# Optimization experiments

Hardware: AMD Instinct MI355X
Metric: run time of the kernel (lower is better)

## Reference

```python
import jax, jax.numpy as jnp
import numpy as np

NUM_ITER = 64
M_CONST = jnp.array([-1.0, 1.0], dtype=jnp.float32)      # constellation m
ALPHA   = jnp.array([0.5, 0.5], dtype=jnp.float32)       # prior alpha


def setup_inputs() -> dict:
    key = jax.random.key(0)
    k1, k2, k3 = jax.random.split(key, 3)
    B, N_RX, N_TX = 16384, 64, 32
    # channel matrix, scaled ~1/sqrt(N_rx) like a normalized MIMO channel
    Ht = jax.random.normal(k1, (B, N_RX, N_TX), dtype=jnp.float32) / jnp.sqrt(jnp.float32(N_RX))
    yt = jax.random.normal(k2, (B, N_RX), dtype=jnp.float32)
    sigmat0 = jax.random.uniform(k3, (B,), dtype=jnp.float32, minval=0.1, maxval=0.6)
    taui = jnp.ones((NUM_ITER + 1,), dtype=jnp.float32)          # taui0 = 1
    delta = jnp.full((NUM_ITER,), 0.01, dtype=jnp.float32)       # small step size for stability
    return {"yt": yt, "Ht": Ht, "sigmat0": sigmat0, "taui": taui, "delta": delta}


def _cmdnet(yt, Ht, sigmat0, taui, delta):
    m = M_CONST                      # [M]
    log_alpha = jnp.log(ALPHA)       # [M]
    sig2 = (sigmat0 ** 2)[:, None, None]          # [B,1,1]
    B, _, K = Ht.shape
    M = m.shape[0]

    # G0 = zeros broadcast to [B, K, M]
    G = jnp.zeros((B, K, M), dtype=Ht.dtype)
    tau = jnp.abs(taui[0])
    ft = jax.nn.softmax((log_alpha + G) * tau, axis=-1)   # [B,K,M]
    xt = jnp.sum(ft * m, axis=-1)                         # [B,K]

    HH = jnp.einsum('bnk,bnl->bkl', Ht, Ht)               # [B,K,K]
    yH = jnp.einsum('bn,bnk->bk', yt, Ht)                 # [B,K]

    def step(carry, xs):
        G, ft, xt, tau = carry
        d_i, tau_next = xs
        xHH = jnp.einsum('bk,bkl->bl', xt, HH)            # [B,K]
        grad_x = tau * (ft * m - ft * xt[..., None])      # [B,K,M]
        grad_L = sig2 * (1.0 - jnp.exp(-G)) + grad_x * (xHH - yH)[..., None]
        G = G - d_i * grad_L
        tau = jnp.abs(tau_next)
        ft = jax.nn.softmax((log_alpha + G) * tau, axis=-1)
        xt = jnp.sum(ft * m, axis=-1)
        return (G, ft, xt, tau), None

    (G, ft, xt, tau), _ = jax.lax.scan(step, (G, ft, xt, tau), (delta, taui[1:]))
    return ft, xt


def reference(yt, Ht, sigmat0, taui, delta):
    return _cmdnet(yt, Ht, sigmat0, taui, delta)
```

## Files before the change

kernel.cpp:

```cpp
#include <hip/hip_runtime.h>


#define NRX 64
#define KSYM 32

typedef float  f32x16 __attribute__((ext_vector_type(16)));
typedef short  short8 __attribute__((ext_vector_type(8)));

__device__ __forceinline__ float readlane_f(float v, int lane) {
    return __int_as_float(__builtin_amdgcn_readlane(__float_as_int(v), lane));
}
__device__ __forceinline__ unsigned cvt_pk_bf16(float a, float b) {
    unsigned r;
    asm("v_cvt_pk_bf16_f32 %0, %1, %2" : "=v"(r) : "v"(a), "v"(b));
    return r;
}
template <int N>
__device__ __forceinline__ float dpp_ror_f(float v) {
    return __int_as_float(__builtin_amdgcn_update_dpp(
        0, __float_as_int(v), 0x120 + N, 0xF, 0xF, true));
}
template <int N>
__device__ __forceinline__ int dpp_ror_i(int v) {
    return __builtin_amdgcn_update_dpp(0, v, 0x120 + N, 0xF, 0xF, true);
}

union FragU { unsigned u[4]; short8 s; };

__global__ __launch_bounds__(256, 4) void cmdnet_kernel(
    const float* __restrict__ yt,
    const float* __restrict__ Ht,
    const float* __restrict__ sigmat0,
    const float* __restrict__ taui,
    const float* __restrict__ delta,
    float* __restrict__ out_ft,
    float* __restrict__ out_xt,
    int niter)
{
    __shared__ __align__(16) float hhbuf[4][KSYM * KSYM];
    __shared__ __align__(16) float ytL[4][2][NRX];

    const int tid  = threadIdx.x;
    const int w    = tid >> 6;
    const int lane = tid & 63;
    const int k    = lane & 31;
    const int h    = lane >> 5;
    const int hi8  = h * 8;
    const int bb   = blockIdx.x * 8 + w * 2;
    const int b    = bb + h;

    ytL[w][0][lane] = yt[(size_t)bb * NRX + lane];
    ytL[w][1][lane] = yt[(size_t)bb * NRX + NRX + lane];

    float dreg = 0.f, treg = 1.f;
    if (lane < niter) { dreg = delta[lane]; treg = fabsf(taui[lane + 1]); }

    float sig2 = sigmat0[b];
    sig2 *= sig2;

    f32x16 acc0, acc1;
    #pragma unroll
    for (int j = 0; j < 16; ++j) { acc0[j] = 0.f; acc1[j] = 0.f; }
    float yhp0 = 0.f, yhp1 = 0.f;

    #pragma unroll
    for (int s = 0; s < 2; ++s) {
        const float* Hb = Ht + ((size_t)(bb + s)) * (NRX * KSYM);
        #pragma unroll
        for (int c = 0; c < 4; ++c) {
            const float* base = Hb + (c * 16 + hi8) * KSYM + k;
            float f[8];
            #pragma unroll
            for (int e = 0; e < 8; ++e) f[e] = base[e * KSYM];

            float4 ya = *reinterpret_cast<const float4*>(&ytL[w][s][c * 16 + hi8]);
            float4 yb = *reinterpret_cast<const float4*>(&ytL[w][s][c * 16 + hi8 + 4]);
            float yp = (s == 0) ? yhp0 : yhp1;
            yp = fmaf(ya.x, f[0], yp); yp = fmaf(ya.y, f[1], yp);
            yp = fmaf(ya.z, f[2], yp); yp = fmaf(ya.w, f[3], yp);
            yp = fmaf(yb.x, f[4], yp); yp = fmaf(yb.y, f[5], yp);
            yp = fmaf(yb.z, f[6], yp); yp = fmaf(yb.w, f[7], yp);
            if (s == 0) yhp0 = yp; else yhp1 = yp;

            FragU hiF, loF;
            #pragma unroll
            for (int p = 0; p < 4; ++p) {
                unsigned hp = cvt_pk_bf16(f[2*p], f[2*p+1]);
                float h0 = __uint_as_float(hp << 16);
                float h1 = __uint_as_float(hp & 0xffff0000u);
                loF.u[p] = cvt_pk_bf16(f[2*p] - h0, f[2*p+1] - h1);
                hiF.u[p] = hp;
            }
            if (s == 0) {
                acc0 = __builtin_amdgcn_mfma_f32_32x32x16_bf16(hiF.s, hiF.s, acc0, 0, 0, 0);
                acc0 = __builtin_amdgcn_mfma_f32_32x32x16_bf16(hiF.s, loF.s, acc0, 0, 0, 0);
                acc0 = __builtin_amdgcn_mfma_f32_32x32x16_bf16(loF.s, hiF.s, acc0, 0, 0, 0);
            } else {
                acc1 = __builtin_amdgcn_mfma_f32_32x32x16_bf16(hiF.s, hiF.s, acc1, 0, 0, 0);
                acc1 = __builtin_amdgcn_mfma_f32_32x32x16_bf16(hiF.s, loF.s, acc1, 0, 0, 0);
                acc1 = __builtin_amdgcn_mfma_f32_32x32x16_bf16(loF.s, hiF.s, acc1, 0, 0, 0);
            }
        }
    }

    float yh0 = yhp0 + __shfl_xor(yhp0, 32, 64);
    float yh1 = yhp1 + __shfl_xor(yhp1, 32, 64);
    float yh  = h ? yh1 : yh0;

    float own_d[32];
    const int low4 = k & 15;
    float* buf = &hhbuf[w][0];
    #pragma unroll
    for (int s = 0; s < 2; ++s) {
        #pragma unroll
        for (int j = 0; j < 16; ++j) {
            int row = (j & 3) + 8 * (j >> 2) + 4 * h;
            buf[row * 32 + k] = s ? acc1[j] : acc0[j];
        }
        if (h == s) {
            const float* rowp = buf + k * 32;
            own_d[0]  = rowp[k];
            own_d[16] = rowp[k ^ 16];
            #define GATH(J) { \
                int idx = dpp_ror_i<J>(low4); \
                own_d[J]        = rowp[(k & 16) | idx]; \
                own_d[16 + (J)] = rowp[((k & 16) ^ 16) | idx]; }
            GATH(1)  GATH(2)  GATH(3)  GATH(4)  GATH(5)
            GATH(6)  GATH(7)  GATH(8)  GATH(9)  GATH(10)
            GATH(11) GATH(12) GATH(13) GATH(14) GATH(15)
            #undef GATH
        }
    }

    float tau = fabsf(taui[0]);
    float G0 = 0.f, G1 = 0.f;
    float ft0 = 0.5f, ft1 = 0.5f, xt = 0.f;

    for (int i = 0; i < niter; ++i) {
        float d        = readlane_f(dreg, i);
        float tau_next = readlane_f(treg, i);

        float xts = __shfl_xor(xt, 16, 64);
        float a[4];
        a[0] = fmaf(own_d[0], xt, -yh);
        a[1] = own_d[16] * xts;
        a[2] = 0.f; a[3] = 0.f;
        #define STEP(J) { \
            float ra = dpp_ror_f<J>(xt); \
            float rb = dpp_ror_f<J>(xts); \
            a[(J) & 3]       = fmaf(own_d[J],        ra, a[(J) & 3]); \
            a[((J) + 2) & 3] = fmaf(own_d[16 + (J)], rb, a[((J) + 2) & 3]); }
        STEP(1)  STEP(2)  STEP(3)  STEP(4)  STEP(5)
        STEP(6)  STEP(7)  STEP(8)  STEP(9)  STEP(10)
        STEP(11) STEP(12) STEP(13) STEP(14) STEP(15)
        #undef STEP
        float r = (a[0] + a[1]) + (a[2] + a[3]);

        float p  = 2.f * tau * ft0 * ft1 * r;
        float e0 = __expf(-G0);
        float e1 = __expf(-G1);
        float g0 = fmaf(sig2, 1.f - e0, -p);
        float g1 = fmaf(sig2, 1.f - e1,  p);
        G0 = fmaf(-d, g0, G0);
        G1 = fmaf(-d, g1, G1);

        tau = tau_next;
        float z  = tau * (G1 - G0);
        float ez = __expf(-fabsf(z));
        float sg = __builtin_amdgcn_rcpf(1.f + ez);
        float abig = sg, asml = ez * sg;
        bool ps = (z >= 0.f);
        ft1 = ps ? abig : asml;
        ft0 = ps ? asml : abig;
        xt  = ft1 - ft0;
    }

    float2 f2 = make_float2(ft0, ft1);
    reinterpret_cast<float2*>(out_ft)[(size_t)b * KSYM + k] = f2;
    out_xt[(size_t)b * KSYM + k] = xt;
}

extern "C" void kernel_launch(void* const* d_in, const int* in_sizes, int n_in,
                              void* d_out, int out_size, void* d_ws, size_t ws_size,
                              hipStream_t stream) {
    const float* yt    = (const float*)d_in[0];
    const float* Ht    = (const float*)d_in[1];
    const float* sg    = (const float*)d_in[2];
    const float* taui  = (const float*)d_in[3];
    const float* delta = (const float*)d_in[4];
    int B     = in_sizes[2];
    int niter = in_sizes[4];
    float* out    = (float*)d_out;
    float* out_ft = out;
    float* out_xt = out + (size_t)B * 64;

    dim3 grid(B / 8), block(256);
    hipLaunchKernelGGL(cmdnet_kernel, grid, block, 0, stream,
                       yt, Ht, sg, taui, delta, out_ft, out_xt, niter);
}
```

Before: 87.74 us.

## Pack Gram matrix to fp16 and use fma_mix in iteration loop

Stores each lane's 32 Gram-matrix entries as 16 packed fp16 pairs and computes the xHH matvec with v_fma_mix_f32, rotating a single packed register per step instead of two floats. It also swaps the shfl_xor for ds_swizzle, rewrites the softmax update in terms of xt alone (ft0*ft1 = (1-xt^2)/4, xt = tanh-like form), and raises the occupancy hint to 8 blocks per CU by scoping the accumulator per batch. This halves register pressure and DPP traffic in the latency-bound loop, at the cost of fp16 rounding of HH and xt, which may affect accuracy over 64 iterations.

```diff
diff --git a/kernel.cpp b/kernel.cpp
--- a/kernel.cpp
+++ b/kernel.cpp
@@ -15,19 +15,21 @@
     asm("v_cvt_pk_bf16_f32 %0, %1, %2" : "=v"(r) : "v"(a), "v"(b));
     return r;
 }
-template <int N>
-__device__ __forceinline__ float dpp_ror_f(float v) {
-    return __int_as_float(__builtin_amdgcn_update_dpp(
-        0, __float_as_int(v), 0x120 + N, 0xF, 0xF, true));
+__device__ __forceinline__ int cvt_pk_f16(float a, float b) {
+    int r;
+    asm("v_cvt_pkrtz_f16_f32 %0, %1, %2" : "=v"(r) : "v"(a), "v"(b));
+    return r;
 }
 template <int N>
 __device__ __forceinline__ int dpp_ror_i(int v) {
     return __builtin_amdgcn_update_dpp(0, v, 0x120 + N, 0xF, 0xF, true);
 }
+#define MIXLO(acc, o, x) asm("v_fma_mix_f32 %0, %1, %2, %0 op_sel:[0,0,0] op_sel_hi:[1,1,0]" : "+v"(acc) : "v"(o), "v"(x))
+#define MIXHI(acc, o, x) asm("v_fma_mix_f32 %0, %1, %2, %0 op_sel:[1,1,0] op_sel_hi:[1,1,0]" : "+v"(acc) : "v"(o), "v"(x))
 
 union FragU { unsigned u[4]; short8 s; };
 
-__global__ __launch_bounds__(256, 4) void cmdnet_kernel(
+__global__ __launch_bounds__(256, 8) void cmdnet_kernel(
     const float* __restrict__ yt,
     const float* __restrict__ Ht,
     const float* __restrict__ sigmat0,
@@ -58,13 +60,17 @@
     float sig2 = sigmat0[b];
     sig2 *= sig2;
 
-    f32x16 acc0, acc1;
-    #pragma unroll
-    for (int j = 0; j < 16; ++j) { acc0[j] = 0.f; acc1[j] = 0.f; }
+    float* buf = &hhbuf[w][0];
+    const int low4 = k & 15;
+    int own_pk[16];
     float yhp0 = 0.f, yhp1 = 0.f;
 
     #pragma unroll
     for (int s = 0; s < 2; ++s) {
+        f32x16 acc;
+        #pragma unroll
+        for (int j = 0; j < 16; ++j) acc[j] = 0.f;
+
         const float* Hb = Ht + ((size_t)(bb + s)) * (NRX * KSYM);
         #pragma unroll
         for (int c = 0; c < 4; ++c) {
@@ -91,15 +97,26 @@
                 loF.u[p] = cvt_pk_bf16(f[2*p] - h0, f[2*p+1] - h1);
                 hiF.u[p] = hp;
             }
-            if (s == 0) {
-                acc0 = __builtin_amdgcn_mfma_f32_32x32x16_bf16(hiF.s, hiF.s, acc0, 0, 0, 0);
-                acc0 = __builtin_amdgcn_mfma_f32_32x32x16_bf16(hiF.s, loF.s, acc0, 0, 0, 0);
-                acc0 = __builtin_amdgcn_mfma_f32_32x32x16_bf16(loF.s, hiF.s, acc0, 0, 0, 0);
-            } else {
-                acc1 = __builtin_amdgcn_mfma_f32_32x32x16_bf16(hiF.s, hiF.s, acc1, 0, 0, 0);
-                acc1 = __builtin_amdgcn_mfma_f32_32x32x16_bf16(hiF.s, loF.s, acc1, 0, 0, 0);
-                acc1 = __builtin_amdgcn_mfma_f32_32x32x16_bf16(loF.s, hiF.s, acc1, 0, 0, 0);
-            }
+            acc = __builtin_amdgcn_mfma_f32_32x32x16_bf16(hiF.s, hiF.s, acc, 0, 0, 0);
+            acc = __builtin_amdgcn_mfma_f32_32x32x16_bf16(hiF.s, loF.s, acc, 0, 0, 0);
+            acc = __builtin_amdgcn_mfma_f32_32x32x16_bf16(loF.s, hiF.s, acc, 0, 0, 0);
+        }
+
+        #pragma unroll
+        for (int j = 0; j < 16; ++j) {
+            int row = (j & 3) + 8 * (j >> 2) + 4 * h;
+            buf[row * 32 + k] = acc[j];
+        }
+        if (h == s) {
+            const float* rowp = buf + k * 32;
+            own_pk[0] = cvt_pk_f16(rowp[k], rowp[k ^ 16]);
+            #define GATH(J) { \
+                int idx = dpp_ror_i<J>(low4); \
+                own_pk[J] = cvt_pk_f16(rowp[(k & 16) | idx], rowp[((k & 16) ^ 16) | idx]); }
+            GATH(1)  GATH(2)  GATH(3)  GATH(4)  GATH(5)
+            GATH(6)  GATH(7)  GATH(8)  GATH(9)  GATH(10)
+            GATH(11) GATH(12) GATH(13) GATH(14) GATH(15)
+            #undef GATH
         }
     }
 
@@ -107,56 +124,33 @@
     float yh1 = yhp1 + __shfl_xor(yhp1, 32, 64);
     float yh  = h ? yh1 : yh0;
 
-    float own_d[32];
-    const int low4 = k & 15;
-    float* buf = &hhbuf[w][0];
-    #pragma unroll
-    for (int s = 0; s < 2; ++s) {
-        #pragma unroll
-        for (int j = 0; j < 16; ++j) {
-            int row = (j & 3) + 8 * (j >> 2) + 4 * h;
-            buf[row * 32 + k] = s ? acc1[j] : acc0[j];
-        }
-        if (h == s) {
-            const float* rowp = buf + k * 32;
-            own_d[0]  = rowp[k];
-            own_d[16] = rowp[k ^ 16];
-            #define GATH(J) { \
-                int idx = dpp_ror_i<J>(low4); \
-                own_d[J]        = rowp[(k & 16) | idx]; \
-                own_d[16 + (J)] = rowp[((k & 16) ^ 16) | idx]; }
-            GATH(1)  GATH(2)  GATH(3)  GATH(4)  GATH(5)
-            GATH(6)  GATH(7)  GATH(8)  GATH(9)  GATH(10)
-            GATH(11) GATH(12) GATH(13) GATH(14) GATH(15)
-            #undef GATH
-        }
-    }
-
     float tau = fabsf(taui[0]);
     float G0 = 0.f, G1 = 0.f;
-    float ft0 = 0.5f, ft1 = 0.5f, xt = 0.f;
+    float xt = 0.f;
 
     for (int i = 0; i < niter; ++i) {
         float d        = readlane_f(dreg, i);
         float tau_next = readlane_f(treg, i);
 
-        float xts = __shfl_xor(xt, 16, 64);
-        float a[4];
-        a[0] = fmaf(own_d[0], xt, -yh);
-        a[1] = own_d[16] * xts;
-        a[2] = 0.f; a[3] = 0.f;
+        float xts = __int_as_float(
+            __builtin_amdgcn_ds_swizzle(__float_as_int(xt), 0x401F));
+        int xpk = cvt_pk_f16(xt, xts);
+
+        float a0 = -yh, a1 = 0.f, a2 = 0.f, a3 = 0.f;
+        MIXLO(a0, own_pk[0], xpk);
+        MIXHI(a1, own_pk[0], xpk);
         #define STEP(J) { \
-            float ra = dpp_ror_f<J>(xt); \
-            float rb = dpp_ror_f<J>(xts); \
-            a[(J) & 3]       = fmaf(own_d[J],        ra, a[(J) & 3]); \
-            a[((J) + 2) & 3] = fmaf(own_d[16 + (J)], rb, a[((J) + 2) & 3]); }
+            int xr = dpp_ror_i<J>(xpk); \
+            if ((J) & 1) { MIXLO(a2, own_pk[J], xr); MIXHI(a3, own_pk[J], xr); } \
+            else         { MIXLO(a0, own_pk[J], xr); MIXHI(a1, own_pk[J], xr); } }
         STEP(1)  STEP(2)  STEP(3)  STEP(4)  STEP(5)
         STEP(6)  STEP(7)  STEP(8)  STEP(9)  STEP(10)
         STEP(11) STEP(12) STEP(13) STEP(14) STEP(15)
         #undef STEP
-        float r = (a[0] + a[1]) + (a[2] + a[3]);
+        float r = (a0 + a2) + (a1 + a3);
 
-        float p  = 2.f * tau * ft0 * ft1 * r;
+        float t  = fmaf(-xt, xt, 1.0f);
+        float p  = 0.5f * tau * t * r;
         float e0 = __expf(-G0);
         float e1 = __expf(-G1);
         float g0 = fmaf(sig2, 1.f - e0, -p);
@@ -168,13 +162,12 @@
         float z  = tau * (G1 - G0);
         float ez = __expf(-fabsf(z));
         float sg = __builtin_amdgcn_rcpf(1.f + ez);
-        float abig = sg, asml = ez * sg;
-        bool ps = (z >= 0.f);
-        ft1 = ps ? abig : asml;
-        ft0 = ps ? asml : abig;
-        xt  = ft1 - ft0;
+        float m  = (1.f - ez) * sg;
+        xt = __builtin_copysignf(m, z);
     }
 
+    float ft1 = fmaf(0.5f, xt, 0.5f);
+    float ft0 = 1.f - ft1;
     float2 f2 = make_float2(ft0, ft1);
     reinterpret_cast<float2*>(out_ft)[(size_t)b * KSYM + k] = f2;
     out_xt[(size_t)b * KSYM + k] = xt;
```

Measured after the change: 164.9 us. +88.0%, slower.
